# Optimization experiments

Hardware: AMD Instinct MI355X
Metric: run time of the kernel (lower is better)

## Reference

```python
import jax, jax.numpy as jnp
import numpy as np


def setup_inputs() -> dict:
    key = jax.random.key(0)
    k1, k2, k3, k4, k5 = jax.random.split(key, 5)
    B, H, N, D = 32, 16, 1024, 128  # batch, heads, max_n_codes, head_dim
    transformer_t_1 = jax.random.normal(k1, (B, H, N, D), dtype=jnp.float32)
    transformer_t = jax.random.normal(k2, (B, H, N, D), dtype=jnp.float32)
    # valid-prefix padding vectors: first L entries nonzero, remainder zero
    lengths = jax.random.randint(k3, (B,), N // 2, N + 1)
    padding_t = (jnp.arange(N)[None, :] < lengths[:, None]).astype(jnp.int32)
    concat_w = jax.random.normal(k4, (1, 2 * D), dtype=jnp.float32) / np.sqrt(2 * D)
    concat_b = jax.random.normal(k5, (1,), dtype=jnp.float32) * 0.01
    return {
        "transformer_t_1": transformer_t_1,
        "transformer_t": transformer_t,
        "padding_t": padding_t,
        "max_n_codes": N,
        "concat_w": concat_w,
        "concat_b": concat_b,
    }


def reference(transformer_t_1, transformer_t, padding_t, max_n_codes, concat_w, concat_b):
    N = max_n_codes
    D = transformer_t.shape[-1]
    # create_padding_matrix: padd = index of first zero in padding row (else N);
    # mask positions n >= padd (True = masked out)
    iszero = padding_t == 0                      # [B, N]
    first0 = jnp.argmax(iszero, axis=1)          # [B]
    padd = jnp.where(iszero.any(axis=1), first0, N)
    mask = (jnp.arange(N)[None, :] >= padd[:, None])[:, None, :]  # [B, 1, N] -> bcast over heads

    # all_nodes_t_1: sum over node dim, broadcast back to every node
    s = transformer_t_1.sum(axis=2)              # [B, H, D]
    # concat Linear([all_nodes, transformer_t]) -> split weight into two halves
    w1 = concat_w[0, :D]
    w2 = concat_w[0, D:]
    score = (jnp.einsum('bhd,d->bh', s, w1)[:, :, None]
             + jnp.einsum('bhnd,d->bhn', transformer_t, w2)
             + concat_b[0])                      # [B, H, N]

    logits = jnp.where(mask, -jnp.inf, score)
    attn = jax.nn.softmax(logits, axis=-1)
    attn = jnp.where(mask, jnp.array(0.0, attn.dtype), attn)

    return transformer_t * attn[..., None] + transformer_t
```

## Files before the change

kernel.cpp:

```cpp
#include <hip/hip_runtime.h>

#define BB 32
#define HH 16
#define NN 1024
#define DD 128

typedef float fvec4 __attribute__((ext_vector_type(4)));

__global__ __launch_bounds__(1024) void fused_kernel(const float* __restrict__ t,
                                                     const int* __restrict__ padding,
                                                     const float* __restrict__ w2,
                                                     float* __restrict__ out) {
    const int bh   = blockIdx.x;
    const int b    = bh >> 4;
    const int tid  = threadIdx.x;
    const int wid  = tid >> 6;
    const int lane = tid & 63;

    __shared__ float s_fac[NN];
    __shared__ int   red_i[16];
    __shared__ float red_f[16];

    const float* trow = t + (long)bh * NN * DD;

    int lm = (padding[b * NN + tid] == 0) ? tid : NN;
#pragma unroll
    for (int off = 32; off; off >>= 1) lm = min(lm, __shfl_xor(lm, off));
    if (lane == 0) red_i[wid] = lm;

    const int hw = tid >> 5;
    const int l  = tid & 31;
    const float4 wv = ((const float4*)w2)[l];
#pragma unroll 4
    for (int it = 0; it < 32; ++it) {
        const int n = hw * 32 + it;
        const float4 tv = ((const float4*)(trow + (long)n * DD))[l];
        float p = tv.x * wv.x + tv.y * wv.y + tv.z * wv.z + tv.w * wv.w;
        p += __shfl_xor(p, 1);
        p += __shfl_xor(p, 2);
        p += __shfl_xor(p, 4);
        p += __shfl_xor(p, 8);
        p += __shfl_xor(p, 16);
        if (l == 0) s_fac[n] = p;
    }
    __syncthreads();

    int padd = NN;
#pragma unroll
    for (int k = 0; k < 16; ++k) padd = min(padd, red_i[k]);

    const float sc  = s_fac[tid];
    const float NEG = -3.4e38f;
    float m = (tid < padd) ? sc : NEG;
#pragma unroll
    for (int off = 32; off; off >>= 1) m = fmaxf(m, __shfl_xor(m, off));
    if (lane == 0) red_f[wid] = m;
    __syncthreads();
    float M = NEG;
#pragma unroll
    for (int k = 0; k < 16; ++k) M = fmaxf(M, red_f[k]);
    __syncthreads();

    const float e = (tid < padd) ? __expf(sc - M) : 0.f;
    float s = e;
#pragma unroll
    for (int off = 32; off; off >>= 1) s += __shfl_xor(s, off);
    if (lane == 0) red_f[wid] = s;
    __syncthreads();
    float S = 0.f;
#pragma unroll
    for (int k = 0; k < 16; ++k) S += red_f[k];

    const float inv = (S > 0.f) ? (1.0f / S) : 0.f;
    s_fac[tid] = 1.f + e * inv;
    __syncthreads();

    const float4* t4 = (const float4*)trow;
    fvec4*        o4 = (fvec4*)(out + (long)bh * NN * DD);
#pragma unroll 4
    for (int it = 0; it < 32; ++it) {
        const int i4 = it * 1024 + tid;
        const float f = s_fac[i4 >> 5];
        float4 v = t4[i4];
        fvec4 nv = {v.x * f, v.y * f, v.z * f, v.w * f};
        __builtin_nontemporal_store(nv, o4 + i4);
    }
}

extern "C" void kernel_launch(void* const* d_in, const int* in_sizes, int n_in,
                              void* d_out, int out_size, void* d_ws, size_t ws_size,
                              hipStream_t stream) {
    const float* t       = (const float*)d_in[1];
    const int*   padding = (const int*)d_in[2];
    const float* cw      = (const float*)d_in[4];
    float*       out     = (float*)d_out;

    fused_kernel<<<BB * HH, 1024, 0, stream>>>(t, padding, cw + DD, out);
}
```

Before: 576.8 us.

## Keep row tiles in registers across softmax to avoid rereading input

Each thread now loads its 32 float4 slices of the tensor once into fully unrolled register variables. It reuses them for both the dot-product scoring pass and the final scaled write, so the second global read of the whole tensor is gone. The 32-lane reduction is restructured to handle two rows per shuffle tree, and launch bounds now request at least 4 waves per EU. The cost is about 128 VGPRs of live data per thread, which risks spills or lower occupancy, and the nontemporal store hint is dropped.

```diff
diff --git a/kernel.cpp b/kernel.cpp
--- a/kernel.cpp
+++ b/kernel.cpp
@@ -5,12 +5,20 @@
 #define NN 1024
 #define DD 128
 
-typedef float fvec4 __attribute__((ext_vector_type(4)));
 
-__global__ __launch_bounds__(1024) void fused_kernel(const float* __restrict__ t,
-                                                     const int* __restrict__ padding,
-                                                     const float* __restrict__ w2,
-                                                     float* __restrict__ out) {
+#define FOR32(M) M(0) M(1) M(2) M(3) M(4) M(5) M(6) M(7) \
+                 M(8) M(9) M(10) M(11) M(12) M(13) M(14) M(15) \
+                 M(16) M(17) M(18) M(19) M(20) M(21) M(22) M(23) \
+                 M(24) M(25) M(26) M(27) M(28) M(29) M(30) M(31)
+
+#define FORPAIRS(M) M(0,1) M(2,3) M(4,5) M(6,7) M(8,9) M(10,11) M(12,13) \
+                    M(14,15) M(16,17) M(18,19) M(20,21) M(22,23) M(24,25) \
+                    M(26,27) M(28,29) M(30,31)
+
+__global__ __launch_bounds__(1024, 4) void fused_kernel(const float* __restrict__ t,
+                                                        const int* __restrict__ padding,
+                                                        const float* __restrict__ w2,
+                                                        float* __restrict__ out) {
     const int bh   = blockIdx.x;
     const int b    = bh >> 4;
     const int tid  = threadIdx.x;
@@ -31,18 +39,34 @@
     const int hw = tid >> 5;
     const int l  = tid & 31;
     const float4 wv = ((const float4*)w2)[l];
-#pragma unroll 4
-    for (int it = 0; it < 32; ++it) {
-        const int n = hw * 32 + it;
-        const float4 tv = ((const float4*)(trow + (long)n * DD))[l];
-        float p = tv.x * wv.x + tv.y * wv.y + tv.z * wv.z + tv.w * wv.w;
-        p += __shfl_xor(p, 1);
-        p += __shfl_xor(p, 2);
-        p += __shfl_xor(p, 4);
-        p += __shfl_xor(p, 8);
-        p += __shfl_xor(p, 16);
-        if (l == 0) s_fac[n] = p;
+    const float4* rowp = (const float4*)(trow + (long)(hw * 32) * DD);
+
+#define DECLV(K) float4 v##K;
+    FOR32(DECLV)
+#undef DECLV
+#define LOADV(K) v##K = rowp[(K) * 32 + l];
+    FOR32(LOADV)
+#undef LOADV
+
+#define PAIR(K0, K1) {                                                        \
+        const float a  = v##K0.x * wv.x + v##K0.y * wv.y                      \
+                       + v##K0.z * wv.z + v##K0.w * wv.w;                     \
+        const float bq = v##K1.x * wv.x + v##K1.y * wv.y                      \
+                       + v##K1.z * wv.z + v##K1.w * wv.w;                     \
+        float x = (l < 16) ? a : bq;                                          \
+        float y = (l < 16) ? bq : a;                                          \
+        x += __shfl_xor(y, 16);                                               \
+        x += __shfl_xor(x, 8);                                                \
+        x += __shfl_xor(x, 4);                                                \
+        x += __shfl_xor(x, 2);                                                \
+        x += __shfl_xor(x, 1);                                                \
+        const int n = hw * 32 + (K0);                                         \
+        if (l == 0)  s_fac[n]     = x;                                        \
+        if (l == 16) s_fac[n + 1] = x;                                        \
     }
+    FORPAIRS(PAIR)
+#undef PAIR
+
     __syncthreads();
 
     int padd = NN;
@@ -75,16 +99,15 @@
     s_fac[tid] = 1.f + e * inv;
     __syncthreads();
 
-    const float4* t4 = (const float4*)trow;
-    fvec4*        o4 = (fvec4*)(out + (long)bh * NN * DD);
-#pragma unroll 4
-    for (int it = 0; it < 32; ++it) {
-        const int i4 = it * 1024 + tid;
-        const float f = s_fac[i4 >> 5];
-        float4 v = t4[i4];
-        fvec4 nv = {v.x * f, v.y * f, v.z * f, v.w * f};
-        __builtin_nontemporal_store(nv, o4 + i4);
+    float4* o4row = (float4*)(out + (long)bh * NN * DD + (long)(hw * 32) * DD);
+#define ST(K) {                                                               \
+        const float f = s_fac[hw * 32 + (K)];                                 \
+        float4 w = v##K;                                                      \
+        w.x *= f; w.y *= f; w.z *= f; w.w *= f;                               \
+        o4row[(K) * 32 + l] = w;                                              \
     }
+    FOR32(ST)
+#undef ST
 }
 
 extern "C" void kernel_launch(void* const* d_in, const int* in_sizes, int n_in,
```

Result: slower. 635.7 us (+10.2%).
